# Performance work log

Hardware: AMD Instinct MI355X
Metric: run time of the kernel (lower is better)

Reference implementation:

```python
import jax, jax.numpy as jnp
import numpy as np
import math

B, S, D, H = 4, 1024, 1024, 16
HD = D // H  # 64
DFF = 4 * D
LN_EPS = 1e-5

def setup_inputs() -> dict:
    key = jax.random.key(0)
    ks = jax.random.split(key, 24)
    sd = lambda fi, fo: 1.0 / math.sqrt(fi)
    def lin(k, fi, fo):
        k1, k2 = jax.random.split(k)
        w = jax.random.uniform(k1, (fi, fo), jnp.float32, -sd(fi, fo), sd(fi, fo))
        b = jax.random.uniform(k2, (fo,), jnp.float32, -sd(fi, fo), sd(fi, fo))
        return w, b
    x = jax.random.normal(ks[0], (B, S, D), jnp.float32)
    Wk, bk = lin(ks[1], D, D)
    Wq, bq = lin(ks[2], D, D)
    Wv, bv = lin(ks[3], D, D)
    # per-head projections stacked over heads: [H, D, HD]
    def head_lin(k):
        kk = jax.random.split(k, H)
        ws, bs = zip(*[lin(kk[h], D, HD) for h in range(H)])
        return jnp.stack(ws), jnp.stack(bs)
    Whq, bhq = head_lin(ks[4])
    Whk, bhk = head_lin(ks[5])
    Whv, bhv = head_lin(ks[6])
    Wo, bo = lin(ks[7], D, D)
    W1, b1 = lin(ks[8], D, DFF)
    W2, b2 = lin(ks[9], DFF, D)
    gamma = jnp.ones((D,), jnp.float32)
    beta = jnp.zeros((D,), jnp.float32)
    return dict(x=x, Wk=Wk, bk=bk, Wq=Wq, bq=bq, Wv=Wv, bv=bv,
                Whq=Whq, bhq=bhq, Whk=Whk, bhk=bhk, Whv=Whv, bhv=bhv,
                Wo=Wo, bo=bo, W1=W1, b1=b1, W2=W2, b2=b2,
                gamma=gamma, beta=beta)

def _layer_norm(x, gamma, beta):
    mu = jnp.mean(x, axis=-1, keepdims=True)
    var = jnp.mean(jnp.square(x - mu), axis=-1, keepdims=True)
    return (x - mu) * jax.lax.rsqrt(var + LN_EPS) * gamma + beta

def reference(x, Wk, bk, Wq, bq, Wv, bv, Whq, bhq, Whk, bhk, Whv, bhv,
              Wo, bo, W1, b1, W2, b2, gamma, beta):
    # outer projections; NOTE: forward passes (k, q, v) into MHA, so the
    # MHA 'Q' stream is k_proj(x), 'K' stream is q_proj(x), 'V' is v_proj(x)
    ko = x @ Wk + bk
    qo = x @ Wq + bq
    vo = x @ Wv + bv
    # per-head projections (batched over heads): [B,H,S,HD]
    q = jnp.einsum('bsd,hde->bhse', ko, Whq) + bhq[None, :, None, :]
    k = jnp.einsum('bsd,hde->bhse', qo, Whk) + bhk[None, :, None, :]
    v = jnp.einsum('bsd,hde->bhse', vo, Whv) + bhv[None, :, None, :]
    # NOTE: original scales by sqrt(d_model), not sqrt(head_dim)
    scores = jnp.einsum('bhse,bhte->bhst', q, k) / math.sqrt(D)
    w = jax.nn.softmax(scores, axis=-1)
    o = jnp.einsum('bhst,bhte->bhse', w, v)         # [B,H,S,HD]
    o = o.transpose(0, 2, 1, 3).reshape(B, S, D)    # concat heads
    attn = o @ Wo + bo
    # dropout is identity in eval; shared LayerNorm after both residuals
    r1 = _layer_norm(x + attn, gamma, beta)
    ff = jax.nn.gelu(r1 @ W1 + b1, approximate=False) @ W2 + b2
    out = _layer_norm(r1 + ff, gamma, beta)
    return out
```

## Files before the change

kernel.cpp:

```cpp
#include <hip/hip_runtime.h>
#include <cstdint>
#include <cstddef>

#define D_MODEL 1024
#define SEQ 1024
#define BATCH 4
#define NHEAD 16
#define HDIM 64
#define ROWS (BATCH*SEQ)

typedef unsigned short u16;
typedef __attribute__((ext_vector_type(4))) unsigned short u16x4;
typedef __attribute__((ext_vector_type(8))) unsigned short u16x8;
typedef __attribute__((ext_vector_type(8))) __bf16 bf16x8v;
typedef __attribute__((ext_vector_type(4))) float f32x4;

__device__ inline u16 f2bf(float f){
  union{float f; unsigned u;} c; c.f = f;
  unsigned r = c.u + 0x7FFFu + ((c.u>>16)&1u);
  return (u16)(r>>16);
}
__device__ inline float bf2f(u16 s){
  union{unsigned u; float f;} c; c.u = ((unsigned)s)<<16; return c.f;
}
__device__ inline float gelu_f(float x){ return 0.5f*x*(1.f+erff(x*0.7071067811865475f)); }

__device__ __forceinline__ void gload_lds16(const void* g, void* l){
  __builtin_amdgcn_global_load_lds(
    (const __attribute__((address_space(1))) unsigned int*)g,
    (__attribute__((address_space(3))) unsigned int*)l, 16, 0, 0);
}

__global__ __launch_bounds__(256) void convert_bf(const float* __restrict__ in, u16* __restrict__ out){
  size_t idx = (size_t)blockIdx.x*256 + threadIdx.x;
  f32x4 v = *(const f32x4*)(in + idx*4);
  u16x4 o = { f2bf(v.x), f2bf(v.y), f2bf(v.z), f2bf(v.w) };
  *(u16x4*)(out + idx*4) = o;
}

__global__ __launch_bounds__(256) void transpose_conv(const float* __restrict__ W, u16* __restrict__ WT, int K, int N){
  __shared__ float tile[32][33];
  int n0 = blockIdx.x*32, k0 = blockIdx.y*32;
  int tx = threadIdx.x & 31, ty = threadIdx.x >> 5;
  #pragma unroll
  for (int i=0;i<4;i++){
    int r = ty + i*8;
    tile[r][tx] = W[(size_t)(k0+r)*N + n0 + tx];
  }
  __syncthreads();
  #pragma unroll
  for (int i=0;i<4;i++){
    int r = ty + i*8;
    WT[(size_t)(n0+r)*K + k0 + tx] = f2bf(tile[tx][r]);
  }
}

__global__ __launch_bounds__(256) void head_transpose(const float* __restrict__ Wh, u16* __restrict__ WT){
  __shared__ float tile[32][33];
  int d0 = blockIdx.x*32, e0 = blockIdx.y*32, h = blockIdx.z;
  int tx = threadIdx.x & 31, ty = threadIdx.x >> 5;
  #pragma unroll
  for (int i=0;i<4;i++){
    int r = ty + i*8;
    tile[r][tx] = Wh[(size_t)h*D_MODEL*HDIM + (size_t)(d0+r)*HDIM + e0 + tx];
  }
  __syncthreads();
  #pragma unroll
  for (int i=0;i<4;i++){
    int r = ty + i*8;
    WT[(size_t)(h*HDIM + e0 + r)*D_MODEL + d0 + tx] = f2bf(tile[tx][r]);
  }
}

__device__ __forceinline__ void gemm_core(u16* As, u16* Bs,
  const u16* __restrict__ A, const u16* __restrict__ BT, const float* __restrict__ bias,
  float* __restrict__ Cf, u16* __restrict__ Cb, int N, int K, int act, int vtrans)
{
  int t = threadIdx.x;
  int lane = t & 63, wid = t >> 6;
  int wr = wid >> 1, wc = wid & 1;
  int fr = lane & 15, kg = lane >> 4;
  int tr = blockIdx.y, tc = blockIdx.x;
  const size_t Abase = (size_t)tr*128*K;
  const size_t Bbase = (size_t)tc*128*K;

  f32x4 acc[4][4];
  #pragma unroll
  for (int m=0;m<4;m++)
    #pragma unroll
    for (int n=0;n<4;n++)
      acc[m][n] = (f32x4)0.f;

  int srow = lane >> 2;
  int sch0 = lane & 3;

  for (int k0 = 0; k0 < K; k0 += 32){
    #pragma unroll
    for (int c=0;c<2;c++){
      int r0 = (wid*2 + c)*16;
      int row = r0 + srow;
      int ch = sch0 ^ ((row >> 1) & 3);
      gload_lds16(A  + Abase + (size_t)row*K + k0 + ch*8, As + r0*32);
      gload_lds16(BT + Bbase + (size_t)row*K + k0 + ch*8, Bs + r0*32);
    }
    __syncthreads();
    bf16x8v af[4], bfv[4];
    #pragma unroll
    for (int m=0;m<4;m++){
      int r = wr*64 + m*16 + fr;
      af[m] = *(const bf16x8v*)&As[r*32 + (kg ^ ((r>>1)&3))*8];
    }
    #pragma unroll
    for (int n=0;n<4;n++){
      int r = wc*64 + n*16 + fr;
      bfv[n] = *(const bf16x8v*)&Bs[r*32 + (kg ^ ((r>>1)&3))*8];
    }
    #pragma unroll
    for (int m=0;m<4;m++)
      #pragma unroll
      for (int n=0;n<4;n++)
        acc[m][n] = __builtin_amdgcn_mfma_f32_16x16x32_bf16(af[m], bfv[n], acc[m][n], 0, 0, 0);
    __syncthreads();
  }

  int crow0 = tr*128 + wr*64;
  int ccol0 = tc*128 + wc*64;
  #pragma unroll
  for (int n=0;n<4;n++){
    int col = ccol0 + n*16 + fr;
    float bv = bias[col];
    #pragma unroll
    for (int m=0;m<4;m++){
      int rbase = crow0 + m*16 + kg*4;
      #pragma unroll
      for (int i=0;i<4;i++){
        float v = acc[m][n][i] + bv;
        if (act) v = gelu_f(v);
        int row = rbase + i;
        if (Cf) Cf[(size_t)row*N + col] = v;
        if (Cb){
          if (vtrans){
            int b = row >> 10, s = row & 1023;
            int h = col >> 6,  e = col & 63;
            Cb[(((size_t)((b*NHEAD + h)*HDIM + e))<<10) + s] = f2bf(v);
          } else {
            Cb[(size_t)row*N + col] = f2bf(v);
          }
        }
      }
    }
  }
}

__global__ __launch_bounds__(256) void gemm1_kernel(
  const u16* A, const u16* BT, const float* bias, float* Cf, u16* Cb, int N, int K, int act)
{
  __shared__ __align__(16) u16 As[128*32];
  __shared__ __align__(16) u16 Bs[128*32];
  gemm_core(As, Bs, A, BT, bias, Cf, Cb, N, K, act, 0);
}

struct B3 { const u16* A[3]; const u16* BT[3]; const float* bias[3]; u16* Cb[3]; int vtrans[3]; };
__global__ __launch_bounds__(256) void gemm3_kernel(B3 p){
  __shared__ __align__(16) u16 As[128*32];
  __shared__ __align__(16) u16 Bs[128*32];
  int z = blockIdx.z;
  gemm_core(As, Bs, p.A[z], p.BT[z], p.bias[z], nullptr, p.Cb[z], D_MODEL, D_MODEL, 0, p.vtrans[z]);
}

__global__ __launch_bounds__(256) void attn_mfma(const u16* __restrict__ Q, const u16* __restrict__ Km,
                                                 const u16* __restrict__ Vt, u16* __restrict__ O)
{
  __shared__ __align__(16) u16 Ks[64*64];
  __shared__ __align__(16) u16 Vs[64*64];
  __shared__ __align__(16) u16 Ps[4][16*64];
  int t = threadIdx.x, lane = t & 63, wid = t >> 6;
  int fr = lane & 15, kg = lane >> 4;
  int qt = blockIdx.x, h = blockIdx.y, b = blockIdx.z;
  const size_t qkbase = ((size_t)b*SEQ)*D_MODEL + (size_t)h*HDIM;
  const size_t vtb = ((size_t)(b*NHEAD + h))*HDIM*SEQ;

  int qrow = qt*64 + wid*16 + fr;
  bf16x8v aq[2];
  aq[0] = *(const bf16x8v*)(Q + qkbase + (size_t)qrow*D_MODEL + kg*8);
  aq[1] = *(const bf16x8v*)(Q + qkbase + (size_t)qrow*D_MODEL + 32 + kg*8);

  f32x4 Oacc[4];
  #pragma unroll
  for (int n=0;n<4;n++) Oacc[n] = (f32x4)0.f;
  float m_run[4], l_run[4];
  #pragma unroll
  for (int i=0;i<4;i++){ m_run[i] = -3e38f; l_run[i] = 0.f; }

  int srow = lane >> 3;
  int sch  = (lane & 7) ^ srow;
  int x7 = fr & 7;

  for (int kt = 0; kt < SEQ/64; ++kt){
    #pragma unroll
    for (int c=0;c<2;c++){
      int r0 = (wid*2 + c)*8;
      int rowk = r0 + srow;
      gload_lds16(Km + qkbase + (size_t)(kt*64 + rowk)*D_MODEL + sch*8, &Ks[r0*64]);
      gload_lds16(Vt + vtb + (size_t)rowk*SEQ + kt*64 + sch*8, &Vs[r0*64]);
    }
    __syncthreads();

    f32x4 z4 = (f32x4)0.f;
    f32x4 s4[4];
    #pragma unroll
    for (int n=0;n<4;n++){
      int r = n*16 + fr;
      bf16x8v k0v = *(const bf16x8v*)&Ks[r*64 + ((kg  ) ^ x7)*8];
      bf16x8v k1v = *(const bf16x8v*)&Ks[r*64 + ((4+kg) ^ x7)*8];
      s4[n] = __builtin_amdgcn_mfma_f32_16x16x32_bf16(aq[0], k0v, z4, 0,0,0);
      s4[n] = __builtin_amdgcn_mfma_f32_16x16x32_bf16(aq[1], k1v, s4[n], 0,0,0);
      s4[n] *= 0.03125f;
    }

    float mI[4], sc[4], ls[4], p[4][4];
    #pragma unroll
    for (int i=0;i<4;i++)
      mI[i] = fmaxf(fmaxf(s4[0][i], s4[1][i]), fmaxf(s4[2][i], s4[3][i]));
    #pragma unroll
    for (int off=1; off<16; off<<=1){
      #pragma unroll
      for (int i=0;i<4;i++) mI[i] = fmaxf(mI[i], __shfl_xor(mI[i], off));
    }
    #pragma unroll
    for (int i=0;i<4;i++){
      float m_new = fmaxf(m_run[i], mI[i]);
      sc[i] = __expf(m_run[i] - m_new);
      m_run[i] = m_new;
      ls[i] = 0.f;
    }
    #pragma unroll
    for (int n=0;n<4;n++)
      #pragma unroll
      for (int i=0;i<4;i++){
        float pv = __expf(s4[n][i] - m_run[i]);
        p[n][i] = pv;
        ls[i] += pv;
      }
    #pragma unroll
    for (int off=1; off<16; off<<=1){
      #pragma unroll
      for (int i=0;i<4;i++) ls[i] += __shfl_xor(ls[i], off);
    }
    #pragma unroll
    for (int i=0;i<4;i++) l_run[i] = l_run[i]*sc[i] + ls[i];
    #pragma unroll
    for (int n=0;n<4;n++)
      #pragma unroll
      for (int i=0;i<4;i++) Oacc[n][i] *= sc[i];

    u16* Pw = &Ps[wid][0];
    #pragma unroll
    for (int n=0;n<4;n++){
      int chunk = n*2 + (fr>>3);
      #pragma unroll
      for (int i=0;i<4;i++){
        int row = kg*4 + i;
        Pw[row*64 + (chunk ^ (row&7))*8 + (fr&7)] = f2bf(p[n][i]);
      }
    }
    asm volatile("s_waitcnt lgkmcnt(0)" ::: "memory");

    bf16x8v ap0 = *(const bf16x8v*)&Pw[fr*64 + ((kg  ) ^ x7)*8];
    bf16x8v ap1 = *(const bf16x8v*)&Pw[fr*64 + ((4+kg) ^ x7)*8];
    #pragma unroll
    for (int n2=0;n2<4;n2++){
      int r = n2*16 + fr;
      bf16x8v v0 = *(const bf16x8v*)&Vs[r*64 + ((kg  ) ^ x7)*8];
      bf16x8v v1 = *(const bf16x8v*)&Vs[r*64 + ((4+kg) ^ x7)*8];
      Oacc[n2] = __builtin_amdgcn_mfma_f32_16x16x32_bf16(ap0, v0, Oacc[n2], 0,0,0);
      Oacc[n2] = __builtin_amdgcn_mfma_f32_16x16x32_bf16(ap1, v1, Oacc[n2], 0,0,0);
    }
    __syncthreads();
  }

  float inv[4];
  #pragma unroll
  for (int i=0;i<4;i++) inv[i] = 1.f / l_run[i];
  #pragma unroll
  for (int n2=0;n2<4;n2++){
    #pragma unroll
    for (int i=0;i<4;i++){
      int row = qt*64 + wid*16 + kg*4 + i;
      O[qkbase + (size_t)row*D_MODEL + n2*16 + fr] = f2bf(Oacc[n2][i]*inv[i]);
    }
  }
}

__global__ __launch_bounds__(256) void ln_kernel(const float* __restrict__ A, const float* __restrict__ B,
   const float* __restrict__ gamma, const float* __restrict__ beta,
   float* __restrict__ Of, u16* __restrict__ Ob)
{
  int row = blockIdx.x, t = threadIdx.x;
  size_t base = (size_t)row*D_MODEL + t*4;
  f32x4 av = *(const f32x4*)(A + base);
  f32x4 bv = *(const f32x4*)(B + base);
  f32x4 v = av + bv;
  float s = v.x+v.y+v.z+v.w;
  float q = v.x*v.x+v.y*v.y+v.z*v.z+v.w*v.w;
  #pragma unroll
  for (int off=1; off<64; off<<=1){ s += __shfl_xor(s,off); q += __shfl_xor(q,off); }
  __shared__ float red[8];
  int wid = t>>6;
  if ((t&63)==0){ red[wid] = s; red[wid+4] = q; }
  __syncthreads();
  s = red[0]+red[1]+red[2]+red[3];
  q = red[4]+red[5]+red[6]+red[7];
  float mu = s*(1.f/1024.f);
  float var = q*(1.f/1024.f) - mu*mu;
  float rs = rsqrtf(var + 1e-5f);
  f32x4 g4 = *(const f32x4*)(gamma + t*4);
  f32x4 b4 = *(const f32x4*)(beta + t*4);
  f32x4 o;
  o.x = (v.x-mu)*rs*g4.x + b4.x;
  o.y = (v.y-mu)*rs*g4.y + b4.y;
  o.z = (v.z-mu)*rs*g4.z + b4.z;
  o.w = (v.w-mu)*rs*g4.w + b4.w;
  *(f32x4*)(Of + base) = o;
  if (Ob){
    u16x4 ob = { f2bf(o.x), f2bf(o.y), f2bf(o.z), f2bf(o.w) };
    *(u16x4*)(Ob + base) = ob;
  }
}

extern "C" void kernel_launch(void* const* d_in, const int* in_sizes, int n_in,
                              void* d_out, int out_size, void* d_ws, size_t ws_size,
                              hipStream_t stream)
{
  const float* x    = (const float*)d_in[0];
  const float* Wk   = (const float*)d_in[1];
  const float* bk   = (const float*)d_in[2];
  const float* Wq   = (const float*)d_in[3];
  const float* bq   = (const float*)d_in[4];
  const float* Wv   = (const float*)d_in[5];
  const float* bv   = (const float*)d_in[6];
  const float* Whq  = (const float*)d_in[7];
  const float* bhq  = (const float*)d_in[8];
  const float* Whk  = (const float*)d_in[9];
  const float* bhk  = (const float*)d_in[10];
  const float* Whv  = (const float*)d_in[11];
  const float* bhv  = (const float*)d_in[12];
  const float* Wo   = (const float*)d_in[13];
  const float* bo   = (const float*)d_in[14];
  const float* W1   = (const float*)d_in[15];
  const float* b1   = (const float*)d_in[16];
  const float* W2   = (const float*)d_in[17];
  const float* b2   = (const float*)d_in[18];
  const float* gamma= (const float*)d_in[19];
  const float* beta = (const float*)d_in[20];

  char* ws = (char*)d_ws;
  const size_t MB_ = 1024*1024;
  u16* WkT  = (u16*)(ws + 0*MB_);
  u16* WqT  = (u16*)(ws + 2*MB_);
  u16* WvT  = (u16*)(ws + 4*MB_);
  u16* WhqT = (u16*)(ws + 6*MB_);
  u16* WhkT = (u16*)(ws + 8*MB_);
  u16* WhvT = (u16*)(ws + 10*MB_);
  u16* WoT  = (u16*)(ws + 12*MB_);
  u16* W1T  = (u16*)(ws + 14*MB_);
  u16* W2T  = (u16*)(ws + 22*MB_);
  u16* xb   = (u16*)(ws + 30*MB_);
  u16* kob  = (u16*)(ws + 38*MB_);
  u16* qob  = (u16*)(ws + 46*MB_);
  u16* vob  = (u16*)(ws + 54*MB_);
  u16* qb   = (u16*)(ws + 62*MB_);
  u16* kb   = (u16*)(ws + 70*MB_);
  u16* vt   = (u16*)(ws + 78*MB_);
  u16* Ob   = (u16*)(ws + 86*MB_);
  float* attn_f = (float*)(ws + 94*MB_);
  float* r1f    = (float*)(ws + 110*MB_);
  u16*  r1b     = (u16*)(ws + 126*MB_);
  u16*  ff1b    = (u16*)(ws + 38*MB_);
  float* ff2f   = (float*)(ws + 94*MB_);

  dim3 tb(256);

  convert_bf<<<dim3(ROWS*D_MODEL/4/256), tb, 0, stream>>>(x, xb);
  transpose_conv<<<dim3(32,32),  tb, 0, stream>>>(Wk, WkT, 1024, 1024);
  transpose_conv<<<dim3(32,32),  tb, 0, stream>>>(Wq, WqT, 1024, 1024);
  transpose_conv<<<dim3(32,32),  tb, 0, stream>>>(Wv, WvT, 1024, 1024);
  transpose_conv<<<dim3(32,32),  tb, 0, stream>>>(Wo, WoT, 1024, 1024);
  transpose_conv<<<dim3(128,32), tb, 0, stream>>>(W1, W1T, 1024, 4096);
  transpose_conv<<<dim3(32,128), tb, 0, stream>>>(W2, W2T, 4096, 1024);
  head_transpose<<<dim3(32,2,16), tb, 0, stream>>>(Whq, WhqT);
  head_transpose<<<dim3(32,2,16), tb, 0, stream>>>(Whk, WhkT);
  head_transpose<<<dim3(32,2,16), tb, 0, stream>>>(Whv, WhvT);

  B3 p1;
  p1.A[0]=xb;  p1.A[1]=xb;  p1.A[2]=xb;
  p1.BT[0]=WkT; p1.BT[1]=WqT; p1.BT[2]=WvT;
  p1.bias[0]=bk; p1.bias[1]=bq; p1.bias[2]=bv;
  p1.Cb[0]=kob; p1.Cb[1]=qob; p1.Cb[2]=vob;
  p1.vtrans[0]=0; p1.vtrans[1]=0; p1.vtrans[2]=0;
  gemm3_kernel<<<dim3(8,32,3), tb, 0, stream>>>(p1);

  B3 p2;
  p2.A[0]=kob; p2.A[1]=qob; p2.A[2]=vob;
  p2.BT[0]=WhqT; p2.BT[1]=WhkT; p2.BT[2]=WhvT;
  p2.bias[0]=bhq; p2.bias[1]=bhk; p2.bias[2]=bhv;
  p2.Cb[0]=qb; p2.Cb[1]=kb; p2.Cb[2]=vt;
  p2.vtrans[0]=0; p2.vtrans[1]=0; p2.vtrans[2]=1;
  gemm3_kernel<<<dim3(8,32,3), tb, 0, stream>>>(p2);

  attn_mfma<<<dim3(16,16,4), tb, 0, stream>>>(qb, kb, vt, Ob);

  gemm1_kernel<<<dim3(8,32), tb, 0, stream>>>(Ob, WoT, bo, attn_f, nullptr, 1024, 1024, 0);
  ln_kernel<<<dim3(4096), tb, 0, stream>>>(x, attn_f, gamma, beta, r1f, r1b);
  gemm1_kernel<<<dim3(32,32), tb, 0, stream>>>(r1b, W1T, b1, nullptr, ff1b, 4096, 1024, 1);
  gemm1_kernel<<<dim3(8,32), tb, 0, stream>>>(ff1b, W2T, b2, ff2f, nullptr, 1024, 4096, 0);
  ln_kernel<<<dim3(4096), tb, 0, stream>>>(r1f, ff2f, gamma, beta, (float*)d_out, nullptr);

  (void)in_sizes; (void)n_in; (void)out_size; (void)ws_size;
}
```

Measured before the change: 376.6 us.

## Double-buffer GEMM K-tiles, use 256x256 tiles for FF1, merge QKV projections

Rewrites the GEMM core to stage 64-wide K tiles into double-buffered, XOR-swizzled LDS. The next tile's global-to-LDS loads are issued before computing on the current one, using explicit vmcnt waits and barriers. The FF1 GEMM gets a new 512-thread kernel with 256x256 output tiles. The three outer Q/K/V projections become one GEMM over a concatenated weight with per-range bias and output routing. The aim is to hide load latency and improve data reuse, at the cost of much more LDS per block (lower occupancy). The merged projection relies on the transposed weights and the output buffers sitting contiguously in the workspace.

```diff
diff --git a/kernel.cpp b/kernel.cpp
--- a/kernel.cpp
+++ b/kernel.cpp
@@ -72,79 +72,190 @@
   }
 }
 
-__device__ __forceinline__ void gemm_core(u16* As, u16* Bs,
+__global__ __launch_bounds__(512) void gemm256(
   const u16* __restrict__ A, const u16* __restrict__ BT, const float* __restrict__ bias,
-  float* __restrict__ Cf, u16* __restrict__ Cb, int N, int K, int act, int vtrans)
+  u16* __restrict__ Cb, int N, int K, int act)
 {
-  int t = threadIdx.x;
-  int lane = t & 63, wid = t >> 6;
-  int wr = wid >> 1, wc = wid & 1;
-  int fr = lane & 15, kg = lane >> 4;
+  __shared__ __align__(16) u16 As[2][256*64];
+  __shared__ __align__(16) u16 Bs[2][256*64];
+  int t = threadIdx.x, lane = t&63, wid = t>>6;
+  int wr = wid>>2, wc = wid&3;
+  int fr = lane&15, kg = lane>>4;
   int tr = blockIdx.y, tc = blockIdx.x;
-  const size_t Abase = (size_t)tr*128*K;
-  const size_t Bbase = (size_t)tc*128*K;
-
-  f32x4 acc[4][4];
-  #pragma unroll
-  for (int m=0;m<4;m++)
-    #pragma unroll
-    for (int n=0;n<4;n++)
-      acc[m][n] = (f32x4)0.f;
-
-  int srow = lane >> 2;
-  int sch0 = lane & 3;
-
-  for (int k0 = 0; k0 < K; k0 += 32){
-    #pragma unroll
-    for (int c=0;c<2;c++){
-      int r0 = (wid*2 + c)*16;
-      int row = r0 + srow;
-      int ch = sch0 ^ ((row >> 1) & 3);
-      gload_lds16(A  + Abase + (size_t)row*K + k0 + ch*8, As + r0*32);
-      gload_lds16(BT + Bbase + (size_t)row*K + k0 + ch*8, Bs + r0*32);
-    }
-    __syncthreads();
-    bf16x8v af[4], bfv[4];
-    #pragma unroll
-    for (int m=0;m<4;m++){
-      int r = wr*64 + m*16 + fr;
-      af[m] = *(const bf16x8v*)&As[r*32 + (kg ^ ((r>>1)&3))*8];
-    }
-    #pragma unroll
-    for (int n=0;n<4;n++){
-      int r = wc*64 + n*16 + fr;
-      bfv[n] = *(const bf16x8v*)&Bs[r*32 + (kg ^ ((r>>1)&3))*8];
-    }
-    #pragma unroll
-    for (int m=0;m<4;m++)
-      #pragma unroll
-      for (int n=0;n<4;n++)
-        acc[m][n] = __builtin_amdgcn_mfma_f32_16x16x32_bf16(af[m], bfv[n], acc[m][n], 0, 0, 0);
-    __syncthreads();
-  }
-
-  int crow0 = tr*128 + wr*64;
-  int ccol0 = tc*128 + wc*64;
+  const u16* Ab = A  + (size_t)tr*256*K;
+  const u16* Bb = BT + (size_t)tc*256*K;
+  int rr = lane>>3, cc = lane&7;
+
+  f32x4 acc[8][4];
+  #pragma unroll
+  for (int m=0;m<8;m++)
+    #pragma unroll
+    for (int n=0;n<4;n++) acc[m][n] = (f32x4)0.f;
+
+  int NT = K >> 6;
+
+  #define STAGE256(buf, kt) { \
+    _Pragma("unroll") \
+    for (int r=0;r<4;r++){ \
+      int reg = r*8 + wid; \
+      int row = reg*8 + rr; \
+      int sch = cc ^ (row&7); \
+      gload_lds16(Ab + (size_t)row*K + (kt)*64 + sch*8, &As[buf][reg*512]); \
+    } \
+    _Pragma("unroll") \
+    for (int r=0;r<4;r++){ \
+      int reg = r*8 + wid; \
+      int row = reg*8 + rr; \
+      int sch = cc ^ (row&7); \
+      gload_lds16(Bb + (size_t)row*K + (kt)*64 + sch*8, &Bs[buf][reg*512]); \
+    } }
+
+  STAGE256(0, 0);
+  for (int kt=0; kt<NT; ++kt){
+    int buf = kt & 1;
+    if (kt+1 < NT){
+      STAGE256(buf^1, kt+1);
+      asm volatile("s_waitcnt vmcnt(8)" ::: "memory");
+    } else {
+      asm volatile("s_waitcnt vmcnt(0)" ::: "memory");
+    }
+    asm volatile("s_barrier" ::: "memory");
+    #pragma unroll
+    for (int ks=0;ks<2;ks++){
+      bf16x8v af[8], bfv[4];
+      #pragma unroll
+      for (int m=0;m<8;m++){
+        int r = wr*128 + m*16 + fr;
+        af[m] = *(const bf16x8v*)&As[buf][r*64 + ((kg+4*ks)^(r&7))*8];
+      }
+      #pragma unroll
+      for (int n=0;n<4;n++){
+        int r = wc*64 + n*16 + fr;
+        bfv[n] = *(const bf16x8v*)&Bs[buf][r*64 + ((kg+4*ks)^(r&7))*8];
+      }
+      #pragma unroll
+      for (int m=0;m<8;m++)
+        #pragma unroll
+        for (int n=0;n<4;n++)
+          acc[m][n] = __builtin_amdgcn_mfma_f32_16x16x32_bf16(af[m], bfv[n], acc[m][n], 0,0,0);
+    }
+    if (kt+1 < NT)
+      asm volatile("s_barrier" ::: "memory");
+  }
+
+  int crow0 = tr*256 + wr*128;
+  int ccol0 = tc*256 + wc*64;
   #pragma unroll
   for (int n=0;n<4;n++){
     int col = ccol0 + n*16 + fr;
     float bv = bias[col];
     #pragma unroll
-    for (int m=0;m<4;m++){
+    for (int m=0;m<8;m++){
       int rbase = crow0 + m*16 + kg*4;
       #pragma unroll
       for (int i=0;i<4;i++){
         float v = acc[m][n][i] + bv;
         if (act) v = gelu_f(v);
+        Cb[(size_t)(rbase+i)*N + col] = f2bf(v);
+      }
+    }
+  }
+}
+
+__device__ __forceinline__ void gemm128_core(u16 (*As)[128*64], u16 (*Bs)[128*64],
+  const u16* __restrict__ A, const u16* __restrict__ BT,
+  const float* b0, const float* b1, const float* b2,
+  float* __restrict__ Cf, u16* __restrict__ Cb, int K, int vtrans)
+{
+  int t = threadIdx.x, lane = t&63, wid = t>>6;
+  int wr = wid>>1, wc = wid&1;
+  int fr = lane&15, kg = lane>>4;
+  int tr = blockIdx.y, tc = blockIdx.x;
+  const u16* Ab = A  + (size_t)tr*128*K;
+  const u16* Bb = BT + (size_t)tc*128*K;
+  int rr = lane>>3, cc = lane&7;
+
+  f32x4 acc[4][4];
+  #pragma unroll
+  for (int m=0;m<4;m++)
+    #pragma unroll
+    for (int n=0;n<4;n++) acc[m][n] = (f32x4)0.f;
+
+  int NT = K >> 6;
+
+  #define STAGE128(buf, kt) { \
+    _Pragma("unroll") \
+    for (int r=0;r<4;r++){ \
+      int reg = r*4 + wid; \
+      int row = reg*8 + rr; \
+      int sch = cc ^ (row&7); \
+      gload_lds16(Ab + (size_t)row*K + (kt)*64 + sch*8, &As[buf][reg*512]); \
+    } \
+    _Pragma("unroll") \
+    for (int r=0;r<4;r++){ \
+      int reg = r*4 + wid; \
+      int row = reg*8 + rr; \
+      int sch = cc ^ (row&7); \
+      gload_lds16(Bb + (size_t)row*K + (kt)*64 + sch*8, &Bs[buf][reg*512]); \
+    } }
+
+  STAGE128(0, 0);
+  for (int kt=0; kt<NT; ++kt){
+    int buf = kt & 1;
+    if (kt+1 < NT){
+      STAGE128(buf^1, kt+1);
+      asm volatile("s_waitcnt vmcnt(8)" ::: "memory");
+    } else {
+      asm volatile("s_waitcnt vmcnt(0)" ::: "memory");
+    }
+    asm volatile("s_barrier" ::: "memory");
+    #pragma unroll
+    for (int ks=0;ks<2;ks++){
+      bf16x8v af[4], bfv[4];
+      #pragma unroll
+      for (int m=0;m<4;m++){
+        int r = wr*64 + m*16 + fr;
+        af[m] = *(const bf16x8v*)&As[buf][r*64 + ((kg+4*ks)^(r&7))*8];
+      }
+      #pragma unroll
+      for (int n=0;n<4;n++){
+        int r = wc*64 + n*16 + fr;
+        bfv[n] = *(const bf16x8v*)&Bs[buf][r*64 + ((kg+4*ks)^(r&7))*8];
+      }
+      #pragma unroll
+      for (int m=0;m<4;m++)
+        #pragma unroll
+        for (int n=0;n<4;n++)
+          acc[m][n] = __builtin_amdgcn_mfma_f32_16x16x32_bf16(af[m], bfv[n], acc[m][n], 0,0,0);
+    }
+    if (kt+1 < NT)
+      asm volatile("s_barrier" ::: "memory");
+  }
+
+  int route = tc >> 3;
+  const float* bp = (route==0) ? b0 : (route==1) ? b1 : b2;
+  int crow0 = tr*128 + wr*64;
+  int ccol0 = tc*128 + wc*64;
+  #pragma unroll
+  for (int n=0;n<4;n++){
+    int col = ccol0 + n*16 + fr;
+    float bv = bp[col & 1023];
+    #pragma unroll
+    for (int m=0;m<4;m++){
+      int rbase = crow0 + m*16 + kg*4;
+      #pragma unroll
+      for (int i=0;i<4;i++){
+        float v = acc[m][n][i] + bv;
         int row = rbase + i;
-        if (Cf) Cf[(size_t)row*N + col] = v;
+        size_t idx = (size_t)(col>>10)*(ROWS*1024) + (size_t)row*1024 + (col&1023);
+        if (Cf) Cf[idx] = v;
         if (Cb){
           if (vtrans){
             int b = row >> 10, s = row & 1023;
-            int h = col >> 6,  e = col & 63;
+            int h = (col&1023) >> 6, e = col & 63;
             Cb[(((size_t)((b*NHEAD + h)*HDIM + e))<<10) + s] = f2bf(v);
           } else {
-            Cb[(size_t)row*N + col] = f2bf(v);
+            Cb[idx] = f2bf(v);
           }
         }
       }
@@ -152,20 +263,22 @@
   }
 }
 
-__global__ __launch_bounds__(256) void gemm1_kernel(
-  const u16* A, const u16* BT, const float* bias, float* Cf, u16* Cb, int N, int K, int act)
+__global__ __launch_bounds__(256) void gemm128_g(
+  const u16* A, const u16* BT, const float* b0, const float* b1, const float* b2,
+  float* Cf, u16* Cb, int K)
 {
-  __shared__ __align__(16) u16 As[128*32];
-  __shared__ __align__(16) u16 Bs[128*32];
-  gemm_core(As, Bs, A, BT, bias, Cf, Cb, N, K, act, 0);
+  __shared__ __align__(16) u16 As[2][128*64];
+  __shared__ __align__(16) u16 Bs[2][128*64];
+  gemm128_core(As, Bs, A, BT, b0, b1, b2, Cf, Cb, K, 0);
 }
 
 struct B3 { const u16* A[3]; const u16* BT[3]; const float* bias[3]; u16* Cb[3]; int vtrans[3]; };
-__global__ __launch_bounds__(256) void gemm3_kernel(B3 p){
-  __shared__ __align__(16) u16 As[128*32];
-  __shared__ __align__(16) u16 Bs[128*32];
+__global__ __launch_bounds__(256) void gemm128_b3(B3 p){
+  __shared__ __align__(16) u16 As[2][128*64];
+  __shared__ __align__(16) u16 Bs[2][128*64];
   int z = blockIdx.z;
-  gemm_core(As, Bs, p.A[z], p.BT[z], p.bias[z], nullptr, p.Cb[z], D_MODEL, D_MODEL, 0, p.vtrans[z]);
+  gemm128_core(As, Bs, p.A[z], p.BT[z], p.bias[z], p.bias[z], p.bias[z],
+               nullptr, p.Cb[z], D_MODEL, p.vtrans[z]);
 }
 
 __global__ __launch_bounds__(256) void attn_mfma(const u16* __restrict__ Q, const u16* __restrict__ Km,
@@ -392,13 +505,7 @@
   head_transpose<<<dim3(32,2,16), tb, 0, stream>>>(Whk, WhkT);
   head_transpose<<<dim3(32,2,16), tb, 0, stream>>>(Whv, WhvT);
 
-  B3 p1;
-  p1.A[0]=xb;  p1.A[1]=xb;  p1.A[2]=xb;
-  p1.BT[0]=WkT; p1.BT[1]=WqT; p1.BT[2]=WvT;
-  p1.bias[0]=bk; p1.bias[1]=bq; p1.bias[2]=bv;
-  p1.Cb[0]=kob; p1.Cb[1]=qob; p1.Cb[2]=vob;
-  p1.vtrans[0]=0; p1.vtrans[1]=0; p1.vtrans[2]=0;
-  gemm3_kernel<<<dim3(8,32,3), tb, 0, stream>>>(p1);
+  gemm128_g<<<dim3(24,32), tb, 0, stream>>>(xb, WkT, bk, bq, bv, nullptr, kob, 1024);
 
   B3 p2;
   p2.A[0]=kob; p2.A[1]=qob; p2.A[2]=vob;
@@ -406,14 +513,14 @@
   p2.bias[0]=bhq; p2.bias[1]=bhk; p2.bias[2]=bhv;
   p2.Cb[0]=qb; p2.Cb[1]=kb; p2.Cb[2]=vt;
   p2.vtrans[0]=0; p2.vtrans[1]=0; p2.vtrans[2]=1;
-  gemm3_kernel<<<dim3(8,32,3), tb, 0, stream>>>(p2);
+  gemm128_b3<<<dim3(8,32,3), tb, 0, stream>>>(p2);
 
   attn_mfma<<<dim3(16,16,4), tb, 0, stream>>>(qb, kb, vt, Ob);
 
-  gemm1_kernel<<<dim3(8,32), tb, 0, stream>>>(Ob, WoT, bo, attn_f, nullptr, 1024, 1024, 0);
+  gemm128_g<<<dim3(8,32), tb, 0, stream>>>(Ob, WoT, bo, bo, bo, attn_f, nullptr, 1024);
   ln_kernel<<<dim3(4096), tb, 0, stream>>>(x, attn_f, gamma, beta, r1f, r1b);
-  gemm1_kernel<<<dim3(32,32), tb, 0, stream>>>(r1b, W1T, b1, nullptr, ff1b, 4096, 1024, 1);
-  gemm1_kernel<<<dim3(8,32), tb, 0, stream>>>(ff1b, W2T, b2, ff2f, nullptr, 1024, 4096, 0);
+  gemm256<<<dim3(16,16), dim3(512), 0, stream>>>(r1b, W1T, b1, ff1b, 4096, 1024, 1);
+  gemm128_g<<<dim3(8,32), tb, 0, stream>>>(ff1b, W2T, b2, b2, b2, ff2f, nullptr, 4096);
   ln_kernel<<<dim3(4096), tb, 0, stream>>>(r1f, ff2f, gamma, beta, (float*)d_out, nullptr);
 
   (void)in_sizes; (void)n_in; (void)out_size; (void)ws_size;
```

After: 375.5 us. No clear change (-0.3%).
